# Performance work log

Hardware: AMD Instinct MI355X
Metric: run time of the kernel (lower is better)

## Reference

```python
import jax, jax.numpy as jnp
from jax import lax
import numpy as np

KH, KW = 9, 9  # box-filter window (kernel=(9,9))
IN_CH = 1


def _box_sum(x):
    # F.conv2d(x, ones([1, in_ch, KH, KW]), stride=1, padding=(4, 4))
    k = jnp.ones((1, IN_CH, KH, KW), x.dtype)
    pad = ((KH - 1) // 2, (KH - 1) // 2), ((KW - 1) // 2, (KW - 1) // 2)
    return lax.conv_general_dilated(
        x, k, window_strides=(1, 1), padding=pad,
        dimension_numbers=("NCHW", "OIHW", "NCHW"))


def setup_inputs() -> dict:
    key = jax.random.key(0)
    k1, k2 = jax.random.split(key)
    B, C, H, W = 32, IN_CH, 512, 512
    inp = jax.random.normal(k1, (B, C, H, W), dtype=jnp.float32)
    tgt = jax.random.uniform(k2, (B, C, H, W), dtype=jnp.float32)
    return {"input": inp, "target": tgt}


def reference(input, target):
    # normalize target from [-1, 1] -> [0, 1]
    t = (target + 1.0) * 0.5
    II = input * input
    TT = t * t
    IT = input * t

    T_sum = _box_sum(t)
    I_sum = _box_sum(input)
    TT_sum = _box_sum(TT)
    II_sum = _box_sum(II)
    IT_sum = _box_sum(IT)

    ksize = float(KH * KW)
    Ihat = I_sum / ksize
    That = T_sum / ksize

    cross = IT_sum - Ihat * T_sum - That * I_sum + That * Ihat * ksize
    T_var = TT_sum - 2.0 * That * T_sum + That * That * ksize
    I_var = II_sum - 2.0 * Ihat * I_sum + Ihat * Ihat * ksize

    cc = cross * cross / (T_var * I_var + 1e-5)
    return -1.0 * jnp.mean(cc)
```

## Files before the change

kernel.cpp:

```cpp
#include <hip/hip_runtime.h>

#define IMG_H 512
#define IMG_W 512
#define N_IMG 32
#define ROWS  4
#define BANDS (IMG_H / ROWS)
#define NPIX  (32.0f * 512.0f * 512.0f)

__device__ __forceinline__ float dl(float x) {
    return __int_as_float(__builtin_amdgcn_update_dpp(
        0, __float_as_int(x), 0x138, 0xf, 0xf, true));
}
__device__ __forceinline__ float dr(float x) {
    return __int_as_float(__builtin_amdgcn_update_dpp(
        0, __float_as_int(x), 0x130, 0xf, 0xf, true));
}

template<bool EDGE>
__device__ __forceinline__ void load8t(const float* __restrict__ ip,
                                       const float* __restrict__ tp,
                                       int r, int c0, float* I, float* T) {
    const int rc = EDGE ? min(max(r, 0), IMG_H - 1) : r;
    const float* irow = ip + (ptrdiff_t)rc * IMG_W + c0;
    const float* trow = tp + (ptrdiff_t)rc * IMG_W + c0;
    float4 a = *(const float4*)(irow);
    float4 b = *(const float4*)(irow + 4);
    float4 c = *(const float4*)(trow);
    float4 d = *(const float4*)(trow + 4);
    I[0]=a.x; I[1]=a.y; I[2]=a.z; I[3]=a.w;
    I[4]=b.x; I[5]=b.y; I[6]=b.z; I[7]=b.w;
    T[0]=c.x; T[1]=c.y; T[2]=c.z; T[3]=c.w;
    T[4]=d.x; T[5]=d.y; T[6]=d.z; T[7]=d.w;
    if (EDGE) {
        const bool v = (r >= 0) && (r < IMG_H);
        #pragma unroll
        for (int j = 0; j < 8; ++j) {
            I[j] = v ? I[j] : 0.0f;
            T[j] = v ? T[j] : -1.0f;
        }
    }
}

__device__ __forceinline__ void slide_lead(const float* LI, const float* LTr,
                                           float* vI, float* vT, float* vII,
                                           float* vTT, float* vIT) {
    #pragma unroll
    for (int j = 0; j < 8; ++j) {
        float li = LI[j];
        float lt = fmaf(LTr[j], 0.5f, 0.5f);
        vI[j]  += li;
        vT[j]  += lt;
        vII[j]  = fmaf(li, li, vII[j]);
        vTT[j]  = fmaf(lt, lt, vTT[j]);
        vIT[j]  = fmaf(li, lt, vIT[j]);
    }
}

__device__ __forceinline__ void slide_full(const float* LI, const float* LTr,
                                           const float* QI, const float* QTr,
                                           float* vI, float* vT, float* vII,
                                           float* vTT, float* vIT) {
    #pragma unroll
    for (int j = 0; j < 8; ++j) {
        float li = LI[j], qi = QI[j];
        float lt = fmaf(LTr[j], 0.5f, 0.5f);
        float qt = fmaf(QTr[j], 0.5f, 0.5f);
        float dI = li - qi, aI = li + qi;
        float dT = lt - qt, aT = lt + qt;
        vI[j]  += dI;
        vT[j]  += dT;
        vII[j]  = fmaf(dI, aI, vII[j]);
        vTT[j]  = fmaf(dT, aT, vTT[j]);
        vIT[j]  = fmaf(li, lt, vIT[j] - qi * qt);
    }
}

__device__ __forceinline__ float cc_of(float sI, float sT, float sII, float sTT, float sIT) {
    const float inv81 = 1.0f / 81.0f;
    float u     = sI * inv81;
    float w     = sT * inv81;
    float cross = fmaf(-u, sT, sIT);
    float iv    = fmaf(-u, sI, sII);
    float tv    = fmaf(-w, sT, sTT);
    float den   = fmaf(tv, iv, 1e-5f);
    return cross * cross * __builtin_amdgcn_rcpf(den);
}

__device__ __forceinline__ float hphase(const float* vI, const float* vT,
                                        const float* vII, const float* vTT,
                                        const float* vIT) {
    float s0 = ((dl(vI [4])+dl(vI [5]))+(dl(vI [6])+dl(vI [7]))) + ((vI [0]+vI [1])+(vI [2]+vI [3])) + vI [4];
    float s1 = ((dl(vT [4])+dl(vT [5]))+(dl(vT [6])+dl(vT [7]))) + ((vT [0]+vT [1])+(vT [2]+vT [3])) + vT [4];
    float s2 = ((dl(vII[4])+dl(vII[5]))+(dl(vII[6])+dl(vII[7]))) + ((vII[0]+vII[1])+(vII[2]+vII[3])) + vII[4];
    float s3 = ((dl(vTT[4])+dl(vTT[5]))+(dl(vTT[6])+dl(vTT[7]))) + ((vTT[0]+vTT[1])+(vTT[2]+vTT[3])) + vTT[4];
    float s4 = ((dl(vIT[4])+dl(vIT[5]))+(dl(vIT[6])+dl(vIT[7]))) + ((vIT[0]+vIT[1])+(vIT[2]+vIT[3])) + vIT[4];
    float part = cc_of(s0, s1, s2, s3, s4);

    #define HSTEP(e0,e1,e2,e3,e4) \
        s0 += (e0); s1 += (e1); s2 += (e2); s3 += (e3); s4 += (e4); \
        part += cc_of(s0, s1, s2, s3, s4);

    HSTEP(vI[5]-dl(vI[4]), vT[5]-dl(vT[4]), vII[5]-dl(vII[4]), vTT[5]-dl(vTT[4]), vIT[5]-dl(vIT[4]))
    HSTEP(vI[6]-dl(vI[5]), vT[6]-dl(vT[5]), vII[6]-dl(vII[5]), vTT[6]-dl(vTT[5]), vIT[6]-dl(vIT[5]))
    HSTEP(vI[7]-dl(vI[6]), vT[7]-dl(vT[6]), vII[7]-dl(vII[6]), vTT[7]-dl(vTT[6]), vIT[7]-dl(vIT[6]))
    HSTEP(dr(vI[0])-dl(vI[7]), dr(vT[0])-dl(vT[7]), dr(vII[0])-dl(vII[7]),
          dr(vTT[0])-dl(vTT[7]), dr(vIT[0])-dl(vIT[7]))
    HSTEP(dr(vI[1])-vI[0], dr(vT[1])-vT[0], dr(vII[1])-vII[0], dr(vTT[1])-vTT[0], dr(vIT[1])-vIT[0])
    HSTEP(dr(vI[2])-vI[1], dr(vT[2])-vT[1], dr(vII[2])-vII[1], dr(vTT[2])-vTT[1], dr(vIT[2])-vIT[1])
    HSTEP(dr(vI[3])-vI[2], dr(vT[3])-vT[2], dr(vII[3])-vII[2], dr(vTT[3])-vTT[2], dr(vIT[3])-vIT[2])
    #undef HSTEP
    return part;
}

template<bool EDGE>
__device__ __forceinline__ float band_body(const float* __restrict__ ip,
                                           const float* __restrict__ tp,
                                           int r0, int c0) {
    float vI[8] = {}, vT[8] = {}, vII[8] = {}, vTT[8] = {}, vIT[8] = {};
    float LI[8], LT[8], QI[8], QT[8];
    float acc = 0.0f;

    #pragma unroll 1
    for (int m = 0; m < 8; ++m) {
        load8t<EDGE>(ip, tp, r0 - 4 + m, c0, LI, LT);
        slide_lead(LI, LT, vI, vT, vII, vTT, vIT);
    }

    load8t<EDGE>(ip, tp, r0 + 4, c0, LI, LT);
    slide_lead(LI, LT, vI, vT, vII, vTT, vIT);
    acc += hphase(vI, vT, vII, vTT, vIT);

    #pragma unroll 1
    for (int m = 9; m < 12; ++m) {
        load8t<EDGE>(ip, tp, r0 + m - 4,  c0, LI, LT);
        load8t<EDGE>(ip, tp, r0 + m - 13, c0, QI, QT);
        slide_full(LI, LT, QI, QT, vI, vT, vII, vTT, vIT);
        acc += hphase(vI, vT, vII, vTT, vIT);
    }
    return acc;
}

__global__ __launch_bounds__(256)
void cc_loss_kernel(const float* __restrict__ in, const float* __restrict__ tg,
                    float* __restrict__ out) {
    __shared__ float red[4];

    const int t    = threadIdx.x;
    const int w    = t >> 6;
    const int lane = t & 63;

    const int bid  = blockIdx.x;
    const int bs   = (bid & 7) * 128 + (bid >> 3);

    const int gband = bs * 4 + w;
    const int b     = gband >> 7;
    const int band  = gband & 127;
    const int r0    = band * ROWS;
    const size_t base = (size_t)b * (IMG_H * IMG_W);
    const float* ip = in + base;
    const float* tp = tg + base;
    const int c0    = lane * 8;

    float acc;
    if (band >= 1 && band <= 126) acc = band_body<false>(ip, tp, r0, c0);
    else                          acc = band_body<true >(ip, tp, r0, c0);

    #pragma unroll
    for (int off = 32; off > 0; off >>= 1) acc += __shfl_down(acc, off, 64);
    if (lane == 0) red[w] = acc;
    __syncthreads();
    if (t == 0)
        atomicAdd(out, (red[0] + red[1] + red[2] + red[3]) * (-1.0f / NPIX));
}

extern "C" void kernel_launch(void* const* d_in, const int* in_sizes, int n_in,
                              void* d_out, int out_size, void* d_ws, size_t ws_size,
                              hipStream_t stream) {
    const float* in = (const float*)d_in[0];
    const float* tg = (const float*)d_in[1];
    float* out = (float*)d_out;

    hipMemsetAsync(out, 0, sizeof(float), stream);
    dim3 grid(N_IMG * BANDS / 4);
    cc_loss_kernel<<<grid, 256, 0, stream>>>(in, tg, out);
}
```

Measured before the change: 117.3 us.

## Double band height and software-pipeline row loads with rotating register buffers

Each wavefront now processes 8 output rows instead of 4, so the 8-row vertical halo is amortized over more outputs and redundant global reads drop. The loop is fully unrolled with six rotating lead-row buffers and two trailing-row buffers, issuing loads several rows ahead of their use to hide memory latency. This raises register pressure, which may reduce occupancy, and halves the number of blocks.

```diff
diff --git a/kernel.cpp b/kernel.cpp
--- a/kernel.cpp
+++ b/kernel.cpp
@@ -3,7 +3,7 @@
 #define IMG_H 512
 #define IMG_W 512
 #define N_IMG 32
-#define ROWS  4
+#define ROWS  8
 #define BANDS (IMG_H / ROWS)
 #define NPIX  (32.0f * 512.0f * 512.0f)
 
@@ -117,26 +117,69 @@
                                            const float* __restrict__ tp,
                                            int r0, int c0) {
     float vI[8] = {}, vT[8] = {}, vII[8] = {}, vTT[8] = {}, vIT[8] = {};
-    float LI[8], LT[8], QI[8], QT[8];
     float acc = 0.0f;
 
-    #pragma unroll 1
-    for (int m = 0; m < 8; ++m) {
-        load8t<EDGE>(ip, tp, r0 - 4 + m, c0, LI, LT);
-        slide_lead(LI, LT, vI, vT, vII, vTT, vIT);
-    }
-
-    load8t<EDGE>(ip, tp, r0 + 4, c0, LI, LT);
-    slide_lead(LI, LT, vI, vT, vII, vTT, vIT);
-    acc += hphase(vI, vT, vII, vTT, vIT);
-
-    #pragma unroll 1
-    for (int m = 9; m < 12; ++m) {
-        load8t<EDGE>(ip, tp, r0 + m - 4,  c0, LI, LT);
-        load8t<EDGE>(ip, tp, r0 + m - 13, c0, QI, QT);
-        slide_full(LI, LT, QI, QT, vI, vT, vII, vTT, vIT);
-        acc += hphase(vI, vT, vII, vTT, vIT);
-    }
+    float AI[8], AT[8], BI[8], BT[8], CI[8], CT[8];
+    float DI[8], DT[8], EI[8], ET[8], FI[8], FT[8];
+    float QI0[8], QT0[8], QI1[8], QT1[8];
+
+    load8t<EDGE>(ip, tp, r0 - 4, c0, AI, AT);
+    load8t<EDGE>(ip, tp, r0 - 3, c0, BI, BT);
+    load8t<EDGE>(ip, tp, r0 - 2, c0, CI, CT);
+    load8t<EDGE>(ip, tp, r0 - 1, c0, DI, DT);
+    load8t<EDGE>(ip, tp, r0 + 0, c0, EI, ET);
+    load8t<EDGE>(ip, tp, r0 + 1, c0, FI, FT);
+
+    slide_lead(AI, AT, vI, vT, vII, vTT, vIT);
+    load8t<EDGE>(ip, tp, r0 + 2, c0, AI, AT);
+    slide_lead(BI, BT, vI, vT, vII, vTT, vIT);
+    load8t<EDGE>(ip, tp, r0 + 3, c0, BI, BT);
+    slide_lead(CI, CT, vI, vT, vII, vTT, vIT);
+    load8t<EDGE>(ip, tp, r0 + 4, c0, CI, CT);
+    slide_lead(DI, DT, vI, vT, vII, vTT, vIT);
+    load8t<EDGE>(ip, tp, r0 + 5, c0, DI, DT);
+    slide_lead(EI, ET, vI, vT, vII, vTT, vIT);
+    load8t<EDGE>(ip, tp, r0 + 6, c0, EI, ET);
+    slide_lead(FI, FT, vI, vT, vII, vTT, vIT);
+    load8t<EDGE>(ip, tp, r0 + 7, c0, FI, FT);
+    slide_lead(AI, AT, vI, vT, vII, vTT, vIT);
+    load8t<EDGE>(ip, tp, r0 + 8, c0, AI, AT);
+    slide_lead(BI, BT, vI, vT, vII, vTT, vIT);
+    load8t<EDGE>(ip, tp, r0 + 9, c0, BI, BT);
+    load8t<EDGE>(ip, tp, r0 - 4, c0, QI0, QT0);
+
+    slide_lead(CI, CT, vI, vT, vII, vTT, vIT);
+    load8t<EDGE>(ip, tp, r0 + 10, c0, CI, CT);
+    load8t<EDGE>(ip, tp, r0 - 3,  c0, QI1, QT1);
+    acc += hphase(vI, vT, vII, vTT, vIT);
+
+    slide_full(DI, DT, QI0, QT0, vI, vT, vII, vTT, vIT);
+    load8t<EDGE>(ip, tp, r0 + 11, c0, DI, DT);
+    load8t<EDGE>(ip, tp, r0 - 2,  c0, QI0, QT0);
+    acc += hphase(vI, vT, vII, vTT, vIT);
+
+    slide_full(EI, ET, QI1, QT1, vI, vT, vII, vTT, vIT);
+    load8t<EDGE>(ip, tp, r0 - 1, c0, QI1, QT1);
+    acc += hphase(vI, vT, vII, vTT, vIT);
+
+    slide_full(FI, FT, QI0, QT0, vI, vT, vII, vTT, vIT);
+    load8t<EDGE>(ip, tp, r0 + 0, c0, QI0, QT0);
+    acc += hphase(vI, vT, vII, vTT, vIT);
+
+    slide_full(AI, AT, QI1, QT1, vI, vT, vII, vTT, vIT);
+    load8t<EDGE>(ip, tp, r0 + 1, c0, QI1, QT1);
+    acc += hphase(vI, vT, vII, vTT, vIT);
+
+    slide_full(BI, BT, QI0, QT0, vI, vT, vII, vTT, vIT);
+    load8t<EDGE>(ip, tp, r0 + 2, c0, QI0, QT0);
+    acc += hphase(vI, vT, vII, vTT, vIT);
+
+    slide_full(CI, CT, QI1, QT1, vI, vT, vII, vTT, vIT);
+    acc += hphase(vI, vT, vII, vTT, vIT);
+
+    slide_full(DI, DT, QI0, QT0, vI, vT, vII, vTT, vIT);
+    acc += hphase(vI, vT, vII, vTT, vIT);
+
     return acc;
 }
 
@@ -150,11 +193,11 @@
     const int lane = t & 63;
 
     const int bid  = blockIdx.x;
-    const int bs   = (bid & 7) * 128 + (bid >> 3);
+    const int bs   = (bid & 7) * 64 + (bid >> 3);
 
     const int gband = bs * 4 + w;
-    const int b     = gband >> 7;
-    const int band  = gband & 127;
+    const int b     = gband >> 6;
+    const int band  = gband & 63;
     const int r0    = band * ROWS;
     const size_t base = (size_t)b * (IMG_H * IMG_W);
     const float* ip = in + base;
@@ -162,8 +205,8 @@
     const int c0    = lane * 8;
 
     float acc;
-    if (band >= 1 && band <= 126) acc = band_body<false>(ip, tp, r0, c0);
-    else                          acc = band_body<true >(ip, tp, r0, c0);
+    if (band >= 1 && band <= 62) acc = band_body<false>(ip, tp, r0, c0);
+    else                         acc = band_body<true >(ip, tp, r0, c0);
 
     #pragma unroll
     for (int off = 32; off > 0; off >>= 1) acc += __shfl_down(acc, off, 64);
```

Measured after the change: 109.0 us. 7.1% less time.

## Double rows per wave band and keep sliding window rows in registers

Applied to the files above, without the earlier changes.

Each wave now handles 8 output rows instead of 4, which cuts the 8-row vertical halo overhead per output row. The ten window rows are loaded up front into named register arrays and then rotated, so the trailing row is reused from registers instead of being reloaded from memory. The separate edge and interior template paths are merged into one path that always clamps and masks. The cost is higher register pressure and lower occupancy, and the grid has half as many blocks.

```diff
diff --git a/kernel.cpp b/kernel.cpp
--- a/kernel.cpp
+++ b/kernel.cpp
@@ -3,7 +3,7 @@
 #define IMG_H 512
 #define IMG_W 512
 #define N_IMG 32
-#define ROWS  4
+#define ROWS  8
 #define BANDS (IMG_H / ROWS)
 #define NPIX  (32.0f * 512.0f * 512.0f)
 
@@ -16,11 +16,10 @@
         0, __float_as_int(x), 0x130, 0xf, 0xf, true));
 }
 
-template<bool EDGE>
-__device__ __forceinline__ void load8t(const float* __restrict__ ip,
+__device__ __forceinline__ void load8c(const float* __restrict__ ip,
                                        const float* __restrict__ tp,
                                        int r, int c0, float* I, float* T) {
-    const int rc = EDGE ? min(max(r, 0), IMG_H - 1) : r;
+    const int rc = min(max(r, 0), IMG_H - 1);
     const float* irow = ip + (ptrdiff_t)rc * IMG_W + c0;
     const float* trow = tp + (ptrdiff_t)rc * IMG_W + c0;
     float4 a = *(const float4*)(irow);
@@ -31,13 +30,11 @@
     I[4]=b.x; I[5]=b.y; I[6]=b.z; I[7]=b.w;
     T[0]=c.x; T[1]=c.y; T[2]=c.z; T[3]=c.w;
     T[4]=d.x; T[5]=d.y; T[6]=d.z; T[7]=d.w;
-    if (EDGE) {
-        const bool v = (r >= 0) && (r < IMG_H);
-        #pragma unroll
-        for (int j = 0; j < 8; ++j) {
-            I[j] = v ? I[j] : 0.0f;
-            T[j] = v ? T[j] : -1.0f;
-        }
+    const bool v = (r >= 0) && (r < IMG_H);
+    #pragma unroll
+    for (int j = 0; j < 8; ++j) {
+        I[j] = v ? I[j] : 0.0f;
+        T[j] = v ? T[j] : -1.0f;
     }
 }
 
@@ -112,31 +109,66 @@
     return part;
 }
 
-template<bool EDGE>
 __device__ __forceinline__ float band_body(const float* __restrict__ ip,
                                            const float* __restrict__ tp,
                                            int r0, int c0) {
     float vI[8] = {}, vT[8] = {}, vII[8] = {}, vTT[8] = {}, vIT[8] = {};
-    float LI[8], LT[8], QI[8], QT[8];
     float acc = 0.0f;
 
-    #pragma unroll 1
-    for (int m = 0; m < 8; ++m) {
-        load8t<EDGE>(ip, tp, r0 - 4 + m, c0, LI, LT);
-        slide_lead(LI, LT, vI, vT, vII, vTT, vIT);
-    }
-
-    load8t<EDGE>(ip, tp, r0 + 4, c0, LI, LT);
-    slide_lead(LI, LT, vI, vT, vII, vTT, vIT);
-    acc += hphase(vI, vT, vII, vTT, vIT);
-
-    #pragma unroll 1
-    for (int m = 9; m < 12; ++m) {
-        load8t<EDGE>(ip, tp, r0 + m - 4,  c0, LI, LT);
-        load8t<EDGE>(ip, tp, r0 + m - 13, c0, QI, QT);
-        slide_full(LI, LT, QI, QT, vI, vT, vII, vTT, vIT);
-        acc += hphase(vI, vT, vII, vTT, vIT);
-    }
+    float S0I[8],S0T[8], S1I[8],S1T[8], S2I[8],S2T[8], S3I[8],S3T[8];
+    float S4I[8],S4T[8], S5I[8],S5T[8], S6I[8],S6T[8];
+    float XAI[8],XAT[8], XBI[8],XBT[8], XCI[8],XCT[8];
+
+    load8c(ip, tp, r0 - 4, c0, S0I, S0T);
+    load8c(ip, tp, r0 - 3, c0, S1I, S1T);
+    load8c(ip, tp, r0 - 2, c0, S2I, S2T);
+    load8c(ip, tp, r0 - 1, c0, S3I, S3T);
+    load8c(ip, tp, r0 + 0, c0, S4I, S4T);
+    load8c(ip, tp, r0 + 1, c0, S5I, S5T);
+    load8c(ip, tp, r0 + 2, c0, S6I, S6T);
+    load8c(ip, tp, r0 + 3, c0, XAI, XAT);
+    load8c(ip, tp, r0 + 4, c0, XBI, XBT);
+    load8c(ip, tp, r0 + 5, c0, XCI, XCT);
+
+    slide_lead(S0I, S0T, vI, vT, vII, vTT, vIT);
+    slide_lead(S1I, S1T, vI, vT, vII, vTT, vIT);
+    slide_lead(S2I, S2T, vI, vT, vII, vTT, vIT);
+    slide_lead(S3I, S3T, vI, vT, vII, vTT, vIT);
+    slide_lead(S4I, S4T, vI, vT, vII, vTT, vIT);
+    slide_lead(S5I, S5T, vI, vT, vII, vTT, vIT);
+    slide_lead(S6I, S6T, vI, vT, vII, vTT, vIT);
+    slide_lead(XAI, XAT, vI, vT, vII, vTT, vIT);
+
+    slide_lead(XBI, XBT, vI, vT, vII, vTT, vIT);
+    acc += hphase(vI, vT, vII, vTT, vIT);
+
+    slide_full(XCI, XCT, S0I, S0T, vI, vT, vII, vTT, vIT);
+    load8c(ip, tp, r0 + 6, c0, S0I, S0T);
+    acc += hphase(vI, vT, vII, vTT, vIT);
+
+    slide_full(S0I, S0T, S1I, S1T, vI, vT, vII, vTT, vIT);
+    load8c(ip, tp, r0 + 7, c0, S1I, S1T);
+    acc += hphase(vI, vT, vII, vTT, vIT);
+
+    slide_full(S1I, S1T, S2I, S2T, vI, vT, vII, vTT, vIT);
+    load8c(ip, tp, r0 + 8, c0, S2I, S2T);
+    acc += hphase(vI, vT, vII, vTT, vIT);
+
+    slide_full(S2I, S2T, S3I, S3T, vI, vT, vII, vTT, vIT);
+    load8c(ip, tp, r0 + 9, c0, S3I, S3T);
+    acc += hphase(vI, vT, vII, vTT, vIT);
+
+    slide_full(S3I, S3T, S4I, S4T, vI, vT, vII, vTT, vIT);
+    load8c(ip, tp, r0 + 10, c0, S4I, S4T);
+    acc += hphase(vI, vT, vII, vTT, vIT);
+
+    slide_full(S4I, S4T, S5I, S5T, vI, vT, vII, vTT, vIT);
+    load8c(ip, tp, r0 + 11, c0, S5I, S5T);
+    acc += hphase(vI, vT, vII, vTT, vIT);
+
+    slide_full(S5I, S5T, S6I, S6T, vI, vT, vII, vTT, vIT);
+    acc += hphase(vI, vT, vII, vTT, vIT);
+
     return acc;
 }
 
@@ -150,20 +182,18 @@
     const int lane = t & 63;
 
     const int bid  = blockIdx.x;
-    const int bs   = (bid & 7) * 128 + (bid >> 3);
+    const int bs   = (bid & 7) * 64 + (bid >> 3);
 
     const int gband = bs * 4 + w;
-    const int b     = gband >> 7;
-    const int band  = gband & 127;
+    const int b     = gband >> 6;
+    const int band  = gband & 63;
     const int r0    = band * ROWS;
     const size_t base = (size_t)b * (IMG_H * IMG_W);
     const float* ip = in + base;
     const float* tp = tg + base;
     const int c0    = lane * 8;
 
-    float acc;
-    if (band >= 1 && band <= 126) acc = band_body<false>(ip, tp, r0, c0);
-    else                          acc = band_body<true >(ip, tp, r0, c0);
+    float acc = band_body(ip, tp, r0, c0);
 
     #pragma unroll
     for (int off = 32; off > 0; off >>= 1) acc += __shfl_down(acc, off, 64);
```

Measured after the change: 103.9 us. -11.4%, faster.
